# Kernel optimization log

Measured on AMD Instinct MI355X. Metric: run time of the kernel, lower is better.

Reference implementation:

```python
import jax, jax.numpy as jnp
import numpy as np
import math

N_LAYERS = 6
F = 512   # num_feature
H = 8     # num_head
DH = F // H
V = 32000 # vocab size
B = 64
S = 512   # == PositionalEncoding max_len
EPS = 1e-5


def _make_pe(max_len, d_model):
    position = np.arange(max_len, dtype=np.float32)[:, None]
    div_term = np.exp(np.arange(0, d_model, 2, dtype=np.float32) * (-math.log(10000.0) / d_model))
    pe = np.zeros((max_len, d_model), dtype=np.float32)
    pe[:, 0::2] = np.sin(position * div_term)
    pe[:, 1::2] = np.cos(position * div_term)
    return jnp.asarray(pe)


def setup_inputs() -> dict:
    key = jax.random.key(0)
    ks = jax.random.split(key, 16)
    w = lambda k, shape, s=0.02: (jax.random.normal(k, shape, dtype=jnp.float32) * s)
    inp = {
        "text": jax.random.randint(ks[0], (B, S), 0, V),
        "emb": jax.random.normal(ks[1], (V, F), dtype=jnp.float32) * 0.25,
        "pe": _make_pe(S, F),
        # per-layer params stacked on leading N axis
        "Wq": w(ks[2], (N_LAYERS, F, F)), "bq": jnp.zeros((N_LAYERS, F), jnp.float32),
        "Wk": w(ks[3], (N_LAYERS, F, F)), "bk": jnp.zeros((N_LAYERS, F), jnp.float32),
        "Wv": w(ks[4], (N_LAYERS, F, F)), "bv": jnp.zeros((N_LAYERS, F), jnp.float32),
        "g1": jnp.ones((N_LAYERS, F), jnp.float32), "beta1": jnp.zeros((N_LAYERS, F), jnp.float32),
        "Wf": w(ks[5], (N_LAYERS, F, F)), "bf": jnp.zeros((N_LAYERS, F), jnp.float32),
        "g2": jnp.ones((N_LAYERS, F), jnp.float32), "beta2": jnp.zeros((N_LAYERS, F), jnp.float32),
    }
    return inp


def _layernorm(x, g, b):
    m = jnp.mean(x, axis=-1, keepdims=True)
    v = jnp.mean(jnp.square(x - m), axis=-1, keepdims=True)
    return (x - m) * jax.lax.rsqrt(v + EPS) * g + b


def _encoder_layer(x, Wq, bq, Wk, bk, Wv, bv, g1, beta1, Wf, bf, g2, beta2):
    Bz, Sz, Fz = x.shape
    q = (x @ Wq + bq).reshape(Bz, Sz, H, DH)
    k = (x @ Wk + bk).reshape(Bz, Sz, H, DH)
    v = (x @ Wv + bv).reshape(Bz, Sz, H, DH)
    # FAITHFUL to source bug: attention over HEADS per token, no 1/sqrt(d) scaling.
    score = jnp.einsum('bshd,bsgd->bshg', q, k)          # [B,S,H,H]
    weight = jax.nn.softmax(score, axis=-1)
    attn = jnp.einsum('bshg,bsgd->bshd', weight, v).reshape(Bz, Sz, Fz)
    x = _layernorm(attn + x, g1, beta1)
    x = _layernorm((x @ Wf + bf) + x, g2, beta2)
    return x


def reference(text, emb, pe, Wq, bq, Wk, bk, Wv, bv, g1, beta1, Wf, bf, g2, beta2):
    x = emb[text] + pe[None, :text.shape[1], :]  # embedding + pos-enc (dropout = eval identity)
    for i in range(N_LAYERS):
        x = _encoder_layer(x, Wq[i], bq[i], Wk[i], bk[i], Wv[i], bv[i],
                           g1[i], beta1[i], Wf[i], bf[i], g2[i], beta2[i])
    return x
```

## Files before the change

kernel.cpp:

```cpp
#include <hip/hip_runtime.h>
#include <stdint.h>

typedef unsigned short u16;
using frag8 = __attribute__((ext_vector_type(8))) short;
using f32x4 = __attribute__((ext_vector_type(4))) float;

#define NTOK 32768
#define FDIM 512

__device__ __forceinline__ float bflo(uint32_t p){ union{uint32_t u; float f;} v; v.u = p<<16; return v.f; }
__device__ __forceinline__ float bfhi(uint32_t p){ union{uint32_t u; float f;} v; v.u = p & 0xffff0000u; return v.f; }
__device__ __forceinline__ float bf1(u16 x){ union{uint32_t u; float f;} v; v.u = ((uint32_t)x)<<16; return v.f; }
__device__ __forceinline__ u16 f2bf(float f){
  union{float f; uint32_t u;} v; v.f = f;
  uint32_t u = v.u;
  u += 0x7fffu + ((u>>16)&1u);
  return (u16)(u>>16);
}

__device__ __forceinline__ void async16(const void* g, void* l){
  __builtin_amdgcn_global_load_lds((const __attribute__((address_space(1))) uint32_t*)g,
                                   (__attribute__((address_space(3))) uint32_t*)l, 16, 0, 0);
}

__global__ __launch_bounds__(256) void embed_kernel(const int* __restrict__ text,
    const float* __restrict__ emb, const float* __restrict__ pe,
    u16* __restrict__ xb, const int tok0){
  const int gid = blockIdx.x*256 + threadIdx.x;
  const int base = gid*4;
  const int tl = base >> 9;
  const int f  = base & 511;
  const int tg = tl + tok0;
  const int s  = tg & 511;
  const int tok = text[tg];
  const float4 e4 = *(const float4*)(emb + (size_t)tok*FDIM + f);
  const float4 p4 = *(const float4*)(pe  + (size_t)s*FDIM + f);
  ushort4 ob;
  ob.x = f2bf(e4.x + p4.x);
  ob.y = f2bf(e4.y + p4.y);
  ob.z = f2bf(e4.z + p4.z);
  ob.w = f2bf(e4.w + p4.w);
  *(ushort4*)(xb + base) = ob;
}

__global__ __launch_bounds__(256) void transpose_w(const float* __restrict__ Wq,
    const float* __restrict__ Wk, const float* __restrict__ Wv, const float* __restrict__ Wf,
    u16* __restrict__ WT){
  const int gid = blockIdx.x*256 + threadIdx.x;
  const int n   = gid & 2047;
  const int k8  = (gid>>11) & 63;
  const int lay = gid >> 17;
  const float* src; int col;
  if      (n <  512){ src = Wq; col = n;      }
  else if (n < 1024){ src = Wk; col = n-512;  }
  else if (n < 1536){ src = Wv; col = n-1024; }
  else              { src = Wf; col = n-1536; }
  src += (size_t)lay*FDIM*FDIM;
  u16 vals[8] __attribute__((aligned(16)));
  #pragma unroll
  for (int i=0;i<8;i++) vals[i] = f2bf(src[(size_t)(k8*8+i)*FDIM + col]);
  *(int4*)(WT + ((size_t)lay*2048 + n)*FDIM + k8*8) = *(const int4*)vals;
}

template<int MODE>
__global__ __launch_bounds__(512, 2) void gemm256(
    const u16* __restrict__ A, const u16* __restrict__ BT,
    const float* __restrict__ b0, const float* __restrict__ b1, const float* __restrict__ b2,
    const u16* __restrict__ resid, u16* __restrict__ C, const int ldC, const int NB){
  __shared__ __attribute__((aligned(16))) short As[4*256*32];
  __shared__ __attribute__((aligned(16))) short Bs[4*256*32];
  const int nwg = gridDim.x;
  const int orig = blockIdx.x;
  const int wg = ((nwg & 7) == 0) ? ((orig & 7)*(nwg >> 3) + (orig >> 3)) : orig;
  const int nblk = wg % NB, mblk = wg / NB;
  const int m0 = mblk << 8, n0 = nblk << 8;
  const int tid = threadIdx.x;
  const int wid = tid >> 6, l = tid & 63;
  const int lm = l & 15, quad = l >> 4;

  const int srow = wid*16 + (l >> 2);
  const int sch  = (l & 3) ^ ((l >> 3) & 3);
  const char* Asrc0 = (const char*)A  + ((size_t)(m0 + srow))*1024 + sch*16;
  const char* Asrc1 = Asrc0 + 128*1024;
  const char* Bsrc0 = (const char*)BT + ((size_t)(n0 + srow))*1024 + sch*16;
  const char* Bsrc1 = Bsrc0 + 128*1024;
  char* ldsAw = (char*)As + wid*1024;
  char* ldsBw = (char*)Bs + wid*1024;

  f32x4 acc[8][4];
  #pragma unroll
  for (int i=0;i<8;i++)
    #pragma unroll
    for (int j=0;j<4;j++){ f32x4 z = {0.f,0.f,0.f,0.f}; acc[i][j] = z; }

  const int rsel = quad ^ ((lm >> 1) & 3);
  const int aB = ((wid>>2)*128 + lm)*32 + rsel*8;
  const int bB = ((wid&3)*64  + lm)*32 + rsel*8;

  #pragma unroll
  for (int kt=0; kt<3; kt++){
    async16(Asrc0 + kt*64, ldsAw + kt*16384);
    async16(Asrc1 + kt*64, ldsAw + kt*16384 + 8192);
    async16(Bsrc0 + kt*64, ldsBw + kt*16384);
    async16(Bsrc1 + kt*64, ldsBw + kt*16384 + 8192);
  }

  for (int t=0; t<16; ++t){
    if (t < 14)       asm volatile("s_waitcnt vmcnt(8)" ::: "memory");
    else if (t == 14) asm volatile("s_waitcnt vmcnt(4)" ::: "memory");
    else              asm volatile("s_waitcnt vmcnt(0)" ::: "memory");
    __builtin_amdgcn_s_barrier();
    asm volatile("" ::: "memory");
    const int slot = t & 3;
    const short* sA = As + slot*8192;
    const short* sB = Bs + slot*8192;
    frag8 af[4], bf[4], ag[4];
    #pragma unroll
    for (int mi=0; mi<4; mi++) af[mi] = *(const frag8*)(sA + aB + mi*512);
    #pragma unroll
    for (int nj=0; nj<4; nj++) bf[nj] = *(const frag8*)(sB + bB + nj*512);
    if (t < 13){
      const int s3 = (t+3) & 3, off = (t+3)*64;
      async16(Asrc0 + off, ldsAw + s3*16384);
      async16(Asrc1 + off, ldsAw + s3*16384 + 8192);
    }
    __builtin_amdgcn_s_setprio(1);
    #pragma unroll
    for (int mi=0; mi<4; mi++)
      #pragma unroll
      for (int nj=0; nj<4; nj++)
        acc[mi][nj] = __builtin_amdgcn_mfma_f32_16x16x32_bf16(af[mi], bf[nj], acc[mi][nj], 0,0,0);
    __builtin_amdgcn_s_setprio(0);
    #pragma unroll
    for (int mi=0; mi<4; mi++) ag[mi] = *(const frag8*)(sA + aB + 2048 + mi*512);
    if (t < 13){
      const int s3 = (t+3) & 3, off = (t+3)*64;
      async16(Bsrc0 + off, ldsBw + s3*16384);
      async16(Bsrc1 + off, ldsBw + s3*16384 + 8192);
    }
    __builtin_amdgcn_s_setprio(1);
    #pragma unroll
    for (int mi=0; mi<4; mi++)
      #pragma unroll
      for (int nj=0; nj<4; nj++)
        acc[4+mi][nj] = __builtin_amdgcn_mfma_f32_16x16x32_bf16(ag[mi], bf[nj], acc[4+mi][nj], 0,0,0);
    __builtin_amdgcn_s_setprio(0);
  }

  float bias[4]; int cols[4];
  #pragma unroll
  for (int nj=0;nj<4;nj++){
    const int c = n0 + (wid&3)*64 + nj*16 + lm;
    cols[nj] = c;
    if (MODE==0) bias[nj] = (c<512 ? b0[c] : (c<1024 ? b1[c-512] : b2[c-1024]));
    else         bias[nj] = b0[c];
  }
  #pragma unroll
  for (int mi=0; mi<8; mi++){
    const int rbase = m0 + (wid>>2)*128 + mi*16 + quad*4;
    #pragma unroll
    for (int r=0;r<4;r++){
      const size_t row = (size_t)(rbase + r);
      #pragma unroll
      for (int nj=0;nj<4;nj++){
        float v = acc[mi][nj][r] + bias[nj];
        if (MODE==1) v += bf1(resid[row*FDIM + cols[nj]]);
        C[row*(size_t)ldC + cols[nj]] = f2bf(v);
      }
    }
  }
}

__global__ __launch_bounds__(256) void attn_ln1(const u16* __restrict__ qkvb,
    const u16* __restrict__ xb, const float* __restrict__ gam, const float* __restrict__ bet,
    u16* __restrict__ y1b){
  __shared__ __attribute__((aligned(16))) u16 sQ[4][1536];
  __shared__ float sWt[4][64];
  const int tid = threadIdx.x, w = tid>>6, l = tid&63;
  const int t = blockIdx.x*4 + w;
  {
    const int4* src = (const int4*)(qkvb + (size_t)t*1536);
    int4* dst = (int4*)(&sQ[w][0]);
    #pragma unroll
    for (int i=0;i<3;i++) dst[i*64 + l] = src[i*64 + l];
  }
  __syncthreads();
  const int h = l>>3, g = l&7;
  const u16* qrow = &sQ[w][h*64];
  const u16* krow = &sQ[w][512 + g*64];
  float sc = 0.f;
  const int dstart = (l&31)*2;
  #pragma unroll
  for (int i=0;i<32;i++){
    const int d = (dstart + 2*i) & 63;
    const uint32_t qp = *(const uint32_t*)(qrow + d);
    const uint32_t kp = *(const uint32_t*)(krow + d);
    sc += bflo(qp)*bflo(kp) + bfhi(qp)*bfhi(kp);
  }
  float mx = sc;
  mx = fmaxf(mx, __shfl_xor(mx,1));
  mx = fmaxf(mx, __shfl_xor(mx,2));
  mx = fmaxf(mx, __shfl_xor(mx,4));
  const float e = __expf(sc - mx);
  float ssum = e;
  ssum += __shfl_xor(ssum,1);
  ssum += __shfl_xor(ssum,2);
  ssum += __shfl_xor(ssum,4);
  sWt[w][l] = e / ssum;
  __syncthreads();
  float wt[8];
  #pragma unroll
  for (int gg=0;gg<8;gg++) wt[gg] = sWt[w][h*8+gg];
  float att[8] = {0,0,0,0,0,0,0,0};
  const int d0 = (l&7)*8;
  #pragma unroll
  for (int gg=0;gg<8;gg++){
    const int4 vv = *(const int4*)(&sQ[w][1024 + gg*64 + d0]);
    const uint32_t* vp = (const uint32_t*)&vv;
    #pragma unroll
    for (int p=0;p<4;p++){
      att[2*p]   += wt[gg]*bflo(vp[p]);
      att[2*p+1] += wt[gg]*bfhi(vp[p]);
    }
  }
  const size_t rb = (size_t)t*FDIM + l*8;
  const int4 xv = *(const int4*)(xb + rb);
  const uint32_t* xp = (const uint32_t*)&xv;
  float y[8]; float s1=0.f, s2=0.f;
  #pragma unroll
  for (int p=0;p<4;p++){
    y[2*p]   = att[2*p]   + bflo(xp[p]);
    y[2*p+1] = att[2*p+1] + bfhi(xp[p]);
  }
  #pragma unroll
  for (int j=0;j<8;j++){ s1 += y[j]; s2 += y[j]*y[j]; }
  #pragma unroll
  for (int off=1; off<64; off<<=1){ s1 += __shfl_xor(s1,off); s2 += __shfl_xor(s2,off); }
  const float mean = s1*(1.f/512.f);
  const float var  = s2*(1.f/512.f) - mean*mean;
  const float rstd = rsqrtf(var + 1e-5f);
  const float4 g0 = *(const float4*)(gam + l*8);
  const float4 g1v = *(const float4*)(gam + l*8 + 4);
  const float4 b0v = *(const float4*)(bet + l*8);
  const float4 b1v = *(const float4*)(bet + l*8 + 4);
  float of[8];
  of[0]=(y[0]-mean)*rstd*g0.x + b0v.x;
  of[1]=(y[1]-mean)*rstd*g0.y + b0v.y;
  of[2]=(y[2]-mean)*rstd*g0.z + b0v.z;
  of[3]=(y[3]-mean)*rstd*g0.w + b0v.w;
  of[4]=(y[4]-mean)*rstd*g1v.x + b1v.x;
  of[5]=(y[5]-mean)*rstd*g1v.y + b1v.y;
  of[6]=(y[6]-mean)*rstd*g1v.z + b1v.z;
  of[7]=(y[7]-mean)*rstd*g1v.w + b1v.w;
  u16 ob[8] __attribute__((aligned(16)));
  #pragma unroll
  for (int j=0;j<8;j++) ob[j] = f2bf(of[j]);
  *(int4*)(y1b + rb) = *(const int4*)ob;
}

__global__ __launch_bounds__(256) void ln2_kernel(const u16* __restrict__ z,
    const float* __restrict__ gam, const float* __restrict__ bet,
    u16* __restrict__ xb, float* __restrict__ outp, const int final_){
  const int tid = threadIdx.x, w = tid>>6, l = tid&63;
  const int t = blockIdx.x*4 + w;
  const size_t rb = (size_t)t*FDIM + l*8;
  const int4 zv = *(const int4*)(z + rb);
  const uint32_t* zp = (const uint32_t*)&zv;
  float y[8];
  #pragma unroll
  for (int p=0;p<4;p++){ y[2*p]=bflo(zp[p]); y[2*p+1]=bfhi(zp[p]); }
  float s1=0.f, s2=0.f;
  #pragma unroll
  for (int j=0;j<8;j++){ s1+=y[j]; s2+=y[j]*y[j]; }
  #pragma unroll
  for (int off=1; off<64; off<<=1){ s1 += __shfl_xor(s1,off); s2 += __shfl_xor(s2,off); }
  const float mean = s1*(1.f/512.f);
  const float var  = s2*(1.f/512.f) - mean*mean;
  const float rstd = rsqrtf(var + 1e-5f);
  const float4 g0 = *(const float4*)(gam + l*8);
  const float4 g1v = *(const float4*)(gam + l*8 + 4);
  const float4 b0v = *(const float4*)(bet + l*8);
  const float4 b1v = *(const float4*)(bet + l*8 + 4);
  float of[8];
  of[0]=(y[0]-mean)*rstd*g0.x + b0v.x;
  of[1]=(y[1]-mean)*rstd*g0.y + b0v.y;
  of[2]=(y[2]-mean)*rstd*g0.z + b0v.z;
  of[3]=(y[3]-mean)*rstd*g0.w + b0v.w;
  of[4]=(y[4]-mean)*rstd*g1v.x + b1v.x;
  of[5]=(y[5]-mean)*rstd*g1v.y + b1v.y;
  of[6]=(y[6]-mean)*rstd*g1v.z + b1v.z;
  of[7]=(y[7]-mean)*rstd*g1v.w + b1v.w;
  if (final_){
    float4 o0; o0.x=of[0]; o0.y=of[1]; o0.z=of[2]; o0.w=of[3];
    float4 o1; o1.x=of[4]; o1.y=of[5]; o1.z=of[6]; o1.w=of[7];
    *(float4*)(outp + rb) = o0;
    *(float4*)(outp + rb + 4) = o1;
  } else {
    u16 ob[8] __attribute__((aligned(16)));
    #pragma unroll
    for (int j=0;j<8;j++) ob[j] = f2bf(of[j]);
    *(int4*)(xb + rb) = *(const int4*)ob;
  }
}

extern "C" void kernel_launch(void* const* d_in, const int* in_sizes, int n_in,
                              void* d_out, int out_size, void* d_ws, size_t ws_size,
                              hipStream_t stream){
  const int*   text = (const int*)d_in[0];
  const float* emb = (const float*)d_in[1];
  const float* pe  = (const float*)d_in[2];
  const float* Wq  = (const float*)d_in[3];
  const float* bq  = (const float*)d_in[4];
  const float* Wk  = (const float*)d_in[5];
  const float* bk  = (const float*)d_in[6];
  const float* Wv  = (const float*)d_in[7];
  const float* bv  = (const float*)d_in[8];
  const float* g1  = (const float*)d_in[9];
  const float* be1 = (const float*)d_in[10];
  const float* Wf  = (const float*)d_in[11];
  const float* bf_ = (const float*)d_in[12];
  const float* g2  = (const float*)d_in[13];
  const float* be2 = (const float*)d_in[14];
  float* outp = (float*)d_out;

  const size_t wtB = (size_t)6*2048*512*2;
  int T = NTOK;
  while (T > 2048 && wtB + (size_t)T*5120 > ws_size) T >>= 1;

  char* ws = (char*)d_ws;
  u16*   WT  = (u16*)ws;
  char*  act = ws + wtB;
  u16*   xb  = (u16*)act;
  u16*   y1b = (u16*)(act + (size_t)T*1024);
  u16*   qkv = (u16*)(act + (size_t)T*2048);
  u16*   zb  = qkv;

  hipLaunchKernelGGL(transpose_w, dim3(3072), dim3(256), 0, stream, Wq, Wk, Wv, Wf, WT);

  const int chunks = NTOK / T;
  for (int c = 0; c < chunks; c++){
    const int tok0 = c*T;
    hipLaunchKernelGGL(embed_kernel, dim3(T/2), dim3(256), 0, stream, text, emb, pe, xb, tok0);
    for (int lay=0; lay<6; lay++){
      const u16* WTl = WT + (size_t)lay*2048*FDIM;
      hipLaunchKernelGGL((gemm256<0>), dim3((T/256)*6), dim3(512), 0, stream,
          xb, WTl, bq + lay*FDIM, bk + lay*FDIM, bv + lay*FDIM, (const u16*)nullptr, qkv, 1536, 6);
      hipLaunchKernelGGL(attn_ln1, dim3(T/4), dim3(256), 0, stream,
          qkv, xb, g1 + lay*FDIM, be1 + lay*FDIM, y1b);
      hipLaunchKernelGGL((gemm256<1>), dim3((T/256)*2), dim3(512), 0, stream,
          y1b, WTl + (size_t)1536*FDIM, bf_ + lay*FDIM, (const float*)nullptr, (const float*)nullptr,
          y1b, zb, 512, 2);
      hipLaunchKernelGGL(ln2_kernel, dim3(T/4), dim3(256), 0, stream,
          zb, g2 + lay*FDIM, be2 + lay*FDIM, xb, outp + (size_t)tok0*FDIM, (lay==5)?1:0);
    }
  }
}
```

Before: 969.0 us.

## Fuse feed-forward GEMM with residual add and LayerNorm2 in one kernel

Replaces the FF gemm256<1> plus separate ln2_kernel with one kernel. Each workgroup computes a full 128x512 row tile, so LayerNorm statistics can be reduced in registers and LDS and the normalized output written directly. This removes the bf16 intermediate z write and re-read and one launch per layer. In exchange, occupancy drops to one workgroup per CU, the pipeline is three stages deep, and only T/128 workgroups run per launch.

```diff
diff --git a/kernel.cpp b/kernel.cpp
--- a/kernel.cpp
+++ b/kernel.cpp
@@ -62,11 +62,10 @@
   *(int4*)(WT + ((size_t)lay*2048 + n)*FDIM + k8*8) = *(const int4*)vals;
 }
 
-template<int MODE>
 __global__ __launch_bounds__(512, 2) void gemm256(
     const u16* __restrict__ A, const u16* __restrict__ BT,
     const float* __restrict__ b0, const float* __restrict__ b1, const float* __restrict__ b2,
-    const u16* __restrict__ resid, u16* __restrict__ C, const int ldC, const int NB){
+    u16* __restrict__ C, const int ldC, const int NB){
   __shared__ __attribute__((aligned(16))) short As[4*256*32];
   __shared__ __attribute__((aligned(16))) short Bs[4*256*32];
   const int nwg = gridDim.x;
@@ -114,11 +113,11 @@
     const int slot = t & 3;
     const short* sA = As + slot*8192;
     const short* sB = Bs + slot*8192;
-    frag8 af[4], bf[4], ag[4];
+    frag8 af[4], bfrg[4], ag[4];
     #pragma unroll
     for (int mi=0; mi<4; mi++) af[mi] = *(const frag8*)(sA + aB + mi*512);
     #pragma unroll
-    for (int nj=0; nj<4; nj++) bf[nj] = *(const frag8*)(sB + bB + nj*512);
+    for (int nj=0; nj<4; nj++) bfrg[nj] = *(const frag8*)(sB + bB + nj*512);
     if (t < 13){
       const int s3 = (t+3) & 3, off = (t+3)*64;
       async16(Asrc0 + off, ldsAw + s3*16384);
@@ -129,7 +128,7 @@
     for (int mi=0; mi<4; mi++)
       #pragma unroll
       for (int nj=0; nj<4; nj++)
-        acc[mi][nj] = __builtin_amdgcn_mfma_f32_16x16x32_bf16(af[mi], bf[nj], acc[mi][nj], 0,0,0);
+        acc[mi][nj] = __builtin_amdgcn_mfma_f32_16x16x32_bf16(af[mi], bfrg[nj], acc[mi][nj], 0,0,0);
     __builtin_amdgcn_s_setprio(0);
     #pragma unroll
     for (int mi=0; mi<4; mi++) ag[mi] = *(const frag8*)(sA + aB + 2048 + mi*512);
@@ -143,7 +142,7 @@
     for (int mi=0; mi<4; mi++)
       #pragma unroll
       for (int nj=0; nj<4; nj++)
-        acc[4+mi][nj] = __builtin_amdgcn_mfma_f32_16x16x32_bf16(ag[mi], bf[nj], acc[4+mi][nj], 0,0,0);
+        acc[4+mi][nj] = __builtin_amdgcn_mfma_f32_16x16x32_bf16(ag[mi], bfrg[nj], acc[4+mi][nj], 0,0,0);
     __builtin_amdgcn_s_setprio(0);
   }
 
@@ -152,8 +151,7 @@
   for (int nj=0;nj<4;nj++){
     const int c = n0 + (wid&3)*64 + nj*16 + lm;
     cols[nj] = c;
-    if (MODE==0) bias[nj] = (c<512 ? b0[c] : (c<1024 ? b1[c-512] : b2[c-1024]));
-    else         bias[nj] = b0[c];
+    bias[nj] = (c<512 ? b0[c] : (c<1024 ? b1[c-512] : b2[c-1024]));
   }
   #pragma unroll
   for (int mi=0; mi<8; mi++){
@@ -164,7 +162,6 @@
       #pragma unroll
       for (int nj=0;nj<4;nj++){
         float v = acc[mi][nj][r] + bias[nj];
-        if (MODE==1) v += bf1(resid[row*FDIM + cols[nj]]);
         C[row*(size_t)ldC + cols[nj]] = f2bf(v);
       }
     }
@@ -258,48 +255,132 @@
   *(int4*)(y1b + rb) = *(const int4*)ob;
 }
 
-__global__ __launch_bounds__(256) void ln2_kernel(const u16* __restrict__ z,
-    const float* __restrict__ gam, const float* __restrict__ bet,
+__global__ __launch_bounds__(512, 1) void gemm_ff_ln2(
+    const u16* __restrict__ y1, const u16* __restrict__ WTf,
+    const float* __restrict__ bfv,
+    const float* __restrict__ g2, const float* __restrict__ be2,
     u16* __restrict__ xb, float* __restrict__ outp, const int final_){
-  const int tid = threadIdx.x, w = tid>>6, l = tid&63;
-  const int t = blockIdx.x*4 + w;
-  const size_t rb = (size_t)t*FDIM + l*8;
-  const int4 zv = *(const int4*)(z + rb);
-  const uint32_t* zp = (const uint32_t*)&zv;
-  float y[8];
-  #pragma unroll
-  for (int p=0;p<4;p++){ y[2*p]=bflo(zp[p]); y[2*p+1]=bfhi(zp[p]); }
-  float s1=0.f, s2=0.f;
-  #pragma unroll
-  for (int j=0;j<8;j++){ s1+=y[j]; s2+=y[j]*y[j]; }
-  #pragma unroll
-  for (int off=1; off<64; off<<=1){ s1 += __shfl_xor(s1,off); s2 += __shfl_xor(s2,off); }
-  const float mean = s1*(1.f/512.f);
-  const float var  = s2*(1.f/512.f) - mean*mean;
-  const float rstd = rsqrtf(var + 1e-5f);
-  const float4 g0 = *(const float4*)(gam + l*8);
-  const float4 g1v = *(const float4*)(gam + l*8 + 4);
-  const float4 b0v = *(const float4*)(bet + l*8);
-  const float4 b1v = *(const float4*)(bet + l*8 + 4);
-  float of[8];
-  of[0]=(y[0]-mean)*rstd*g0.x + b0v.x;
-  of[1]=(y[1]-mean)*rstd*g0.y + b0v.y;
-  of[2]=(y[2]-mean)*rstd*g0.z + b0v.z;
-  of[3]=(y[3]-mean)*rstd*g0.w + b0v.w;
-  of[4]=(y[4]-mean)*rstd*g1v.x + b1v.x;
-  of[5]=(y[5]-mean)*rstd*g1v.y + b1v.y;
-  of[6]=(y[6]-mean)*rstd*g1v.z + b1v.z;
-  of[7]=(y[7]-mean)*rstd*g1v.w + b1v.w;
-  if (final_){
-    float4 o0; o0.x=of[0]; o0.y=of[1]; o0.z=of[2]; o0.w=of[3];
-    float4 o1; o1.x=of[4]; o1.y=of[5]; o1.z=of[6]; o1.w=of[7];
-    *(float4*)(outp + rb) = o0;
-    *(float4*)(outp + rb + 4) = o1;
-  } else {
-    u16 ob[8] __attribute__((aligned(16)));
-    #pragma unroll
-    for (int j=0;j<8;j++) ob[j] = f2bf(of[j]);
-    *(int4*)(xb + rb) = *(const int4*)ob;
+  __shared__ __attribute__((aligned(16))) short As[3*128*32];
+  __shared__ __attribute__((aligned(16))) short Bs[3*512*32];
+  __shared__ float ln2S[128*8];
+  const int m0 = blockIdx.x << 7;
+  const int tid = threadIdx.x;
+  const int wid = tid>>6, l = tid&63;
+  const int lm = l&15, quad = l>>4;
+  const int wm = wid>>2, wn = wid&3;
+
+  const int srow = wid*16 + (l>>2);
+  const int sch  = (l&3) ^ ((l>>3)&3);
+  const char* Asrc = (const char*)y1  + ((size_t)(m0 + srow))*1024 + sch*16;
+  const char* Bsrc = (const char*)WTf + ((size_t)srow)*1024 + sch*16;
+  char* ldsAw = (char*)As + wid*1024;
+  char* ldsBw = (char*)Bs + wid*1024;
+
+  f32x4 acc[4][8];
+  #pragma unroll
+  for (int i=0;i<4;i++)
+    #pragma unroll
+    for (int j=0;j<8;j++){ f32x4 z = {0.f,0.f,0.f,0.f}; acc[i][j] = z; }
+
+  const int rsel = quad ^ ((lm>>1)&3);
+  const int aB = (wm*64  + lm)*32 + rsel*8;
+  const int bB = (wn*128 + lm)*32 + rsel*8;
+
+  #pragma unroll
+  for (int kt=0; kt<2; kt++){
+    async16(Asrc + kt*64, ldsAw + kt*8192);
+    #pragma unroll
+    for (int r=0;r<4;r++)
+      async16(Bsrc + (size_t)r*131072 + kt*64, ldsBw + kt*32768 + r*8192);
+  }
+
+#define FT(T_, DOSTAGE, VMC) { \
+    asm volatile("s_waitcnt vmcnt(" #VMC ")" ::: "memory"); \
+    __builtin_amdgcn_s_barrier(); \
+    asm volatile("" ::: "memory"); \
+    if (DOSTAGE){ const int s_=((T_)+2)%3; const int off_=((T_)+2)*64; \
+      async16(Asrc + off_, ldsAw + s_*8192); \
+      _Pragma("unroll") \
+      for (int r_=0;r_<4;r_++) \
+        async16(Bsrc + (size_t)r_*131072 + off_, ldsBw + s_*32768 + r_*8192); } \
+    const short* sA_ = As + ((T_)%3)*4096; \
+    const short* sB_ = Bs + ((T_)%3)*16384; \
+    frag8 af_[4], bf_[8]; \
+    _Pragma("unroll") \
+    for (int x_=0;x_<4;x_++) af_[x_] = *(const frag8*)(sA_ + aB + x_*512); \
+    _Pragma("unroll") \
+    for (int x_=0;x_<8;x_++) bf_[x_] = *(const frag8*)(sB_ + bB + x_*512); \
+    __builtin_amdgcn_s_setprio(1); \
+    _Pragma("unroll") \
+    for (int mi_=0;mi_<4;mi_++) \
+      _Pragma("unroll") \
+      for (int nj_=0;nj_<8;nj_++) \
+        acc[mi_][nj_] = __builtin_amdgcn_mfma_f32_16x16x32_bf16(af_[mi_], bf_[nj_], acc[mi_][nj_], 0,0,0); \
+    __builtin_amdgcn_s_setprio(0); }
+
+  FT(0,1,5)  FT(1,1,5)  FT(2,1,5)  FT(3,1,5)
+  FT(4,1,5)  FT(5,1,5)  FT(6,1,5)  FT(7,1,5)
+  FT(8,1,5)  FT(9,1,5)  FT(10,1,5) FT(11,1,5)
+  FT(12,1,5) FT(13,1,5) FT(14,0,5) FT(15,0,0)
+#undef FT
+
+  int cols[8]; float bia[8], gg2[8], bb2[8];
+  #pragma unroll
+  for (int nj=0;nj<8;nj++){
+    const int c = wn*128 + nj*16 + lm;
+    cols[nj] = c; bia[nj] = bfv[c]; gg2[nj] = g2[c]; bb2[nj] = be2[c];
+  }
+  #pragma unroll
+  for (int mi=0;mi<4;mi++){
+    #pragma unroll
+    for (int r=0;r<4;r++){
+      const int row_l = wm*64 + mi*16 + quad*4 + r;
+      const size_t rg = (size_t)(m0 + row_l)*FDIM;
+      #pragma unroll
+      for (int nj=0;nj<8;nj++)
+        acc[mi][nj][r] += bia[nj] + bf1(y1[rg + cols[nj]]);
+    }
+  }
+  #pragma unroll
+  for (int mi=0;mi<4;mi++){
+    #pragma unroll
+    for (int r=0;r<4;r++){
+      const int row_l = wm*64 + mi*16 + quad*4 + r;
+      float s1 = 0.f, s2 = 0.f;
+      #pragma unroll
+      for (int nj=0;nj<8;nj++){ const float v = acc[mi][nj][r]; s1 += v; s2 += v*v; }
+      s1 += __shfl_xor(s1,1); s2 += __shfl_xor(s2,1);
+      s1 += __shfl_xor(s1,2); s2 += __shfl_xor(s2,2);
+      s1 += __shfl_xor(s1,4); s2 += __shfl_xor(s2,4);
+      s1 += __shfl_xor(s1,8); s2 += __shfl_xor(s2,8);
+      if (lm == 0){
+        ln2S[row_l*8 + wn*2]     = s1;
+        ln2S[row_l*8 + wn*2 + 1] = s2;
+      }
+    }
+  }
+  __syncthreads();
+  #pragma unroll
+  for (int mi=0;mi<4;mi++){
+    #pragma unroll
+    for (int r=0;r<4;r++){
+      const int row_l = wm*64 + mi*16 + quad*4 + r;
+      const float s1t = ln2S[row_l*8] + ln2S[row_l*8+2] + ln2S[row_l*8+4] + ln2S[row_l*8+6];
+      const float s2t = ln2S[row_l*8+1] + ln2S[row_l*8+3] + ln2S[row_l*8+5] + ln2S[row_l*8+7];
+      const float mean = s1t*(1.f/512.f);
+      const float var  = s2t*(1.f/512.f) - mean*mean;
+      const float rstd = rsqrtf(var + 1e-5f);
+      const size_t rg = (size_t)(m0 + row_l)*FDIM;
+      if (final_){
+        #pragma unroll
+        for (int nj=0;nj<8;nj++)
+          outp[rg + cols[nj]] = (acc[mi][nj][r]-mean)*rstd*gg2[nj] + bb2[nj];
+      } else {
+        #pragma unroll
+        for (int nj=0;nj<8;nj++)
+          xb[rg + cols[nj]] = f2bf((acc[mi][nj][r]-mean)*rstd*gg2[nj] + bb2[nj]);
+      }
+    }
   }
 }
 
@@ -333,7 +414,6 @@
   u16*   xb  = (u16*)act;
   u16*   y1b = (u16*)(act + (size_t)T*1024);
   u16*   qkv = (u16*)(act + (size_t)T*2048);
-  u16*   zb  = qkv;
 
   hipLaunchKernelGGL(transpose_w, dim3(3072), dim3(256), 0, stream, Wq, Wk, Wv, Wf, WT);
 
@@ -343,15 +423,14 @@
     hipLaunchKernelGGL(embed_kernel, dim3(T/2), dim3(256), 0, stream, text, emb, pe, xb, tok0);
     for (int lay=0; lay<6; lay++){
       const u16* WTl = WT + (size_t)lay*2048*FDIM;
-      hipLaunchKernelGGL((gemm256<0>), dim3((T/256)*6), dim3(512), 0, stream,
-          xb, WTl, bq + lay*FDIM, bk + lay*FDIM, bv + lay*FDIM, (const u16*)nullptr, qkv, 1536, 6);
+      hipLaunchKernelGGL(gemm256, dim3((T/256)*6), dim3(512), 0, stream,
+          xb, WTl, bq + lay*FDIM, bk + lay*FDIM, bv + lay*FDIM, qkv, 1536, 6);
       hipLaunchKernelGGL(attn_ln1, dim3(T/4), dim3(256), 0, stream,
           qkv, xb, g1 + lay*FDIM, be1 + lay*FDIM, y1b);
-      hipLaunchKernelGGL((gemm256<1>), dim3((T/256)*2), dim3(512), 0, stream,
-          y1b, WTl + (size_t)1536*FDIM, bf_ + lay*FDIM, (const float*)nullptr, (const float*)nullptr,
-          y1b, zb, 512, 2);
-      hipLaunchKernelGGL(ln2_kernel, dim3(T/4), dim3(256), 0, stream,
-          zb, g2 + lay*FDIM, be2 + lay*FDIM, xb, outp + (size_t)tok0*FDIM, (lay==5)?1:0);
-    }
-  }
-}
+      hipLaunchKernelGGL(gemm_ff_ln2, dim3(T/128), dim3(512), 0, stream,
+          y1b, WTl + (size_t)1536*FDIM, bf_ + lay*FDIM,
+          g2 + lay*FDIM, be2 + lay*FDIM,
+          xb, outp + (size_t)tok0*FDIM, (lay==5)?1:0);
+    }
+  }
+}
```

Measured after the change: 1.111 ms. +14.7%, slower.
